# Optimization experiments

Measured on AMD Instinct MI355X. Metric: run time of the kernel, lower is better.

## Reference

```python
import jax, jax.numpy as jnp
import numpy as np

E = 1024
H = 16
D = E // H  # head_dim = 64
B = 2
S = 2048


def setup_inputs() -> dict:
    key = jax.random.key(0)
    ks = jax.random.split(key, 8)
    sc = 0.02
    return {
        "x": jax.random.normal(ks[0], (B, S, E), jnp.float32),
        "rotation_params": jax.random.normal(ks[1], (E, E), jnp.float32) * sc,
        "entangle_params": jax.random.normal(ks[2], (E, E), jnp.float32) * sc,
        "qkv_w": jax.random.normal(ks[3], (3 * E, E), jnp.float32) * sc,
        "qkv_b": jax.random.normal(ks[4], (3 * E,), jnp.float32) * sc,
        "out_w": jax.random.normal(ks[5], (E, E), jnp.float32) * sc,
        "out_b": jax.random.normal(ks[6], (E,), jnp.float32) * sc,
    }


def reference(x, rotation_params, entangle_params, qkv_w, qkv_b, out_w, out_b):
    b, s, _ = x.shape
    # qkv projection (torch Linear: x @ W.T + b)
    qkv = jnp.einsum('bse,fe->bsf', x, qkv_w) + qkv_b
    q, k, v = jnp.split(qkv, 3, axis=-1)
    # extra rotation / entangle matmuls on q and k
    q = jnp.matmul(q, rotation_params)
    k = jnp.matmul(k, entangle_params)
    # split heads: (b, h, s, d)
    q = q.reshape(b, s, H, D).transpose(0, 2, 1, 3)
    k = k.reshape(b, s, H, D).transpose(0, 2, 1, 3)
    v = v.reshape(b, s, H, D).transpose(0, 2, 1, 3)
    scores = jnp.einsum('bhqd,bhkd->bhqk', q, k) / np.sqrt(D).astype(np.float32)
    attn = jax.nn.softmax(scores, axis=-1)  # dropout p=0.0 -> identity
    out = jnp.einsum('bhqk,bhkd->bhqd', attn, v)
    out = out.transpose(0, 2, 1, 3).reshape(b, s, E)
    out = jnp.einsum('bse,fe->bsf', out, out_w) + out_b
    return out + x
```

## Files before the change

kernel.cpp:

```cpp
#include <hip/hip_runtime.h>

#define US unsigned short
#define UC unsigned char

typedef __bf16 bf16x8 __attribute__((ext_vector_type(8)));
typedef float f32x4 __attribute__((ext_vector_type(4)));
typedef unsigned int u32x4 __attribute__((ext_vector_type(4)));
typedef unsigned short u16x4 __attribute__((ext_vector_type(4)));
typedef unsigned int uint2v __attribute__((ext_vector_type(2)));

#define ALPHA_Q 0.180336880111f

#if __has_builtin(__builtin_amdgcn_exp2f)
#define EXP2F(x) __builtin_amdgcn_exp2f(x)
#else
#define EXP2F(x) __expf(0.69314718f * (x))
#endif

static __device__ __forceinline__ US f2bf(float f) {
    union { float f; unsigned u; } v; v.f = f;
    unsigned r = v.u + 0x7fffu + ((v.u >> 16) & 1u);
    return (US)(r >> 16);
}
static __device__ __forceinline__ float bf2f(US h) {
    union { unsigned u; float f; } v; v.u = ((unsigned)h) << 16;
    return v.f;
}
static __device__ __forceinline__ f32x4 mfma16(bf16x8 a, bf16x8 b, f32x4 c) {
    return __builtin_amdgcn_mfma_f32_16x16x32_bf16(a, b, c, 0, 0, 0);
}
static __device__ __forceinline__ f32x4 mfma_fp8(long long a, long long b, f32x4 c) {
    return __builtin_amdgcn_mfma_f32_16x16x32_fp8_fp8(a, b, c, 0, 0, 0);
}
static __device__ __forceinline__ void gload16(const US* g, US* l) {
    __builtin_amdgcn_global_load_lds(
        (const __attribute__((address_space(1))) void*)g,
        (__attribute__((address_space(3))) void*)l, 16, 0, 0);
}
static __device__ __forceinline__ void gload16b(const UC* g, UC* l) {
    __builtin_amdgcn_global_load_lds(
        (const __attribute__((address_space(1))) void*)g,
        (__attribute__((address_space(3))) void*)l, 16, 0, 0);
}
static __device__ __forceinline__ void stf(float* p, float v) { *p = v; }
static __device__ __forceinline__ void stf(US* p, float v) { *p = f2bf(v); }

__global__ __launch_bounds__(256) void prep(
    const float* __restrict__ x, US* __restrict__ xb,
    const float* __restrict__ qkvw, US* __restrict__ wv,
    const float* __restrict__ outw, US* __restrict__ wo,
    const float* __restrict__ Rm, US* __restrict__ rt,
    const float* __restrict__ Em, US* __restrict__ et,
    US* __restrict__ wqT, US* __restrict__ wkT,
    const float* __restrict__ qkvb, float* __restrict__ b3)
{
    __shared__ float t[64][65];
    const int bx = blockIdx.x;
    if (bx < 6144) {
        int i = bx * 256 + threadIdx.x;
        const float* s; US* d; int j;
        if (i < 1048576) { s = x; d = xb; j = i; }
        else if (i < 1310720) { s = qkvw + (size_t)2048 * 1024; d = wv; j = i - 1048576; }
        else { s = outw; d = wo; j = i - 1310720; }
        f32x4 v = ((const f32x4*)s)[j];
        u16x4 o;
        o.x = f2bf(v.x); o.y = f2bf(v.y); o.z = f2bf(v.z); o.w = f2bf(v.w);
        ((u16x4*)d)[j] = o;
    } else if (bx < 7168) {
        int r = bx - 6144;
        int z = r >> 8, xy = r & 255, tbx = xy & 15, tby = xy >> 4;
        const float* ip; US* op;
        switch (z) {
            case 0: ip = Rm; op = rt; break;
            case 1: ip = Em; op = et; break;
            case 2: ip = qkvw; op = wqT; break;
            default: ip = qkvw + (size_t)1024 * 1024; op = wkT; break;
        }
        int bc = tbx * 64, br = tby * 64;
        int lx = threadIdx.x & 63, y4 = threadIdx.x >> 6;
#pragma unroll
        for (int i = 0; i < 16; ++i) {
            int rr = i * 4 + y4;
            t[rr][lx] = ip[(size_t)(br + rr) * 1024 + bc + lx];
        }
        __syncthreads();
#pragma unroll
        for (int i = 0; i < 16; ++i) {
            int c = i * 4 + y4;
            op[(size_t)(bc + c) * 1024 + br + lx] = f2bf(t[lx][c]);
        }
    } else if (bx < 7296) {
        float (*red)[64] = (float(*)[64])t;
        const int bb = bx - 7168;
        const int tid = threadIdx.x, wave = tid >> 6, lane = tid & 63;
        const int nc = bb & 31, jc = bb >> 5;
        const int n0 = nc * 64, n = n0 + lane;
        const float* M = (n0 < 1024) ? Rm : Em;
        const float* bv = qkvb + ((n0 < 1024) ? 0 : 1024);
        const int nn = (n0 < 1024) ? n : n - 1024;
        float s = 0.f;
        const int j0 = jc * 256 + wave * 64;
#pragma unroll 8
        for (int j = 0; j < 64; ++j)
            s += bv[j0 + j] * M[(size_t)(j0 + j) * 1024 + nn];
        red[wave][lane] = s;
        __syncthreads();
        if (wave == 0) {
            float tt = red[0][lane] + red[1][lane] + red[2][lane] + red[3][lane];
            atomicAdd(&b3[n], (n0 < 1024) ? tt * ALPHA_Q : tt);
        }
    } else {
        int i = (bx - 7296) * 256 + threadIdx.x;
        b3[2048 + i] = qkvb[2048 + i];
    }
}

template <typename TO>
__global__ __launch_bounds__(256) void gemm_nt64(
    const US* __restrict__ A, const US* __restrict__ Bm,
    TO* __restrict__ C, const float* __restrict__ bias,
    const float* __restrict__ resid,
    int M, int N, int K, int lda, int ldb, int ldc)
{
    __shared__ __align__(16) US sA[64 * 64];
    __shared__ __align__(16) US sB[128 * 64];
    const int tid = threadIdx.x;
    const int wave = tid >> 6, lane = tid & 63;
    const int r16 = lane & 15, q4 = lane >> 4;
    const int wm = (wave >> 1) * 32, wn = (wave & 1) * 64;
    const int c7 = r16 & 7;

    const int l8 = lane >> 3, lg = (lane & 7) ^ l8;
    const US* aptr = A + (size_t)(blockIdx.x * 64 + wave * 16 + l8) * lda + lg * 8;
    const US* bptr = Bm + (size_t)(blockIdx.y * 128 + wave * 32 + l8) * ldb + lg * 8;

    f32x4 acc[2][4];
#pragma unroll
    for (int i = 0; i < 2; ++i)
#pragma unroll
        for (int j = 0; j < 4; ++j) acc[i][j] = (f32x4){0.f, 0.f, 0.f, 0.f};

    for (int k0 = 0; k0 < K; k0 += 64) {
        gload16(aptr + k0, sA + (wave * 16) * 64);
        gload16(aptr + (size_t)8 * lda + k0, sA + (wave * 16 + 8) * 64);
#pragma unroll
        for (int c = 0; c < 4; ++c)
            gload16(bptr + (size_t)(c * 8) * ldb + k0, sB + (wave * 32 + c * 8) * 64);
        __syncthreads();
        bf16x8 af[2][2], bfr[4][2];
#pragma unroll
        for (int i = 0; i < 2; ++i)
#pragma unroll
            for (int hf = 0; hf < 2; ++hf)
                af[i][hf] = *(const bf16x8*)&sA[(wm + i * 16 + r16) * 64 + ((hf * 4 + q4) ^ c7) * 8];
#pragma unroll
        for (int j = 0; j < 4; ++j)
#pragma unroll
            for (int hf = 0; hf < 2; ++hf)
                bfr[j][hf] = *(const bf16x8*)&sB[(wn + j * 16 + r16) * 64 + ((hf * 4 + q4) ^ c7) * 8];
#pragma unroll
        for (int i = 0; i < 2; ++i)
#pragma unroll
            for (int j = 0; j < 4; ++j) {
                acc[i][j] = mfma16(af[i][0], bfr[j][0], acc[i][j]);
                acc[i][j] = mfma16(af[i][1], bfr[j][1], acc[i][j]);
            }
        __syncthreads();
    }

#pragma unroll
    for (int j = 0; j < 4; ++j) {
        int col = blockIdx.y * 128 + wn + j * 16 + r16;
        float bv = bias ? bias[col] : 0.f;
#pragma unroll
        for (int i = 0; i < 2; ++i) {
#pragma unroll
            for (int rr = 0; rr < 4; ++rr) {
                int row = blockIdx.x * 64 + wm + i * 16 + q4 * 4 + rr;
                float v = acc[i][j][rr] + bv;
                if (resid) v += resid[(size_t)row * ldc + col];
                stf(&C[(size_t)row * ldc + col], v);
            }
        }
    }
}

__global__ __launch_bounds__(256) void gemm_qkv(
    const US* __restrict__ A, const US* __restrict__ Bm,
    const float* __restrict__ bias,
    US* __restrict__ qk, UC* __restrict__ vt)
{
    __shared__ __align__(16) US sA[64 * 64];
    __shared__ __align__(16) US sB[128 * 64];
    const int tid = threadIdx.x;
    const int wave = tid >> 6, lane = tid & 63;
    const int r16 = lane & 15, q4 = lane >> 4;
    const int wm = (wave >> 1) * 32, wn = (wave & 1) * 64;
    const int c7 = r16 & 7;

    const int l8 = lane >> 3, lg = (lane & 7) ^ l8;
    const US* aptr = A + (size_t)(blockIdx.x * 64 + wave * 16 + l8) * 1024 + lg * 8;
    const US* bptr = Bm + (size_t)(blockIdx.y * 128 + wave * 32 + l8) * 1024 + lg * 8;

    f32x4 acc[2][4];
#pragma unroll
    for (int i = 0; i < 2; ++i)
#pragma unroll
        for (int j = 0; j < 4; ++j) acc[i][j] = (f32x4){0.f, 0.f, 0.f, 0.f};

    for (int k0 = 0; k0 < 1024; k0 += 64) {
        gload16(aptr + k0, sA + (wave * 16) * 64);
        gload16(aptr + (size_t)8 * 1024 + k0, sA + (wave * 16 + 8) * 64);
#pragma unroll
        for (int c = 0; c < 4; ++c)
            gload16(bptr + (size_t)(c * 8) * 1024 + k0, sB + (wave * 32 + c * 8) * 64);
        __syncthreads();
        bf16x8 af[2][2], bfr[4][2];
#pragma unroll
        for (int i = 0; i < 2; ++i)
#pragma unroll
            for (int hf = 0; hf < 2; ++hf)
                af[i][hf] = *(const bf16x8*)&sA[(wm + i * 16 + r16) * 64 + ((hf * 4 + q4) ^ c7) * 8];
#pragma unroll
        for (int j = 0; j < 4; ++j)
#pragma unroll
            for (int hf = 0; hf < 2; ++hf)
                bfr[j][hf] = *(const bf16x8*)&sB[(wn + j * 16 + r16) * 64 + ((hf * 4 + q4) ^ c7) * 8];
#pragma unroll
        for (int i = 0; i < 2; ++i)
#pragma unroll
            for (int j = 0; j < 4; ++j) {
                acc[i][j] = mfma16(af[i][0], bfr[j][0], acc[i][j]);
                acc[i][j] = mfma16(af[i][1], bfr[j][1], acc[i][j]);
            }
        __syncthreads();
    }

    if (blockIdx.y < 16) {
#pragma unroll
        for (int j = 0; j < 4; ++j) {
            int col = blockIdx.y * 128 + wn + j * 16 + r16;
            float bv = bias[col];
#pragma unroll
            for (int i = 0; i < 2; ++i)
#pragma unroll
                for (int rr = 0; rr < 4; ++rr) {
                    int row = blockIdx.x * 64 + wm + i * 16 + q4 * 4 + rr;
                    qk[(size_t)row * 2048 + col] = f2bf(acc[i][j][rr] + bv);
                }
        }
    } else {
#pragma unroll
        for (int j = 0; j < 4; ++j) {
            int col = blockIdx.y * 128 + wn + j * 16 + r16;
            float bv = bias[col];
            int f = col - 2048;
#pragma unroll
            for (int i = 0; i < 2; ++i) {
                int row0 = blockIdx.x * 64 + wm + i * 16 + q4 * 4;
                int b = row0 >> 11, s0 = row0 & 2047;
                int k = s0 & 63;
                int p = (s0 & ~63) | ((k & 24) << 1) | ((k & 32) >> 2) | (k & 7);
                int dw = __builtin_amdgcn_cvt_pk_fp8_f32(
                    acc[i][j][0] + bv, acc[i][j][1] + bv, 0, false);
                dw = __builtin_amdgcn_cvt_pk_fp8_f32(
                    acc[i][j][2] + bv, acc[i][j][3] + bv, dw, true);
                *(unsigned int*)&vt[((size_t)(b * 1024 + f)) * 2048 + p] = (unsigned)dw;
            }
        }
    }
}

__global__ __launch_bounds__(256) void gemm_fold(
    const US* __restrict__ rt, const US* __restrict__ wqT,
    const US* __restrict__ et, const US* __restrict__ wkT,
    US* __restrict__ comb)
{
    __shared__ __align__(16) US sA[64 * 32];
    __shared__ __align__(16) US sB[64 * 32];
    const US* A; const US* Bm; US* C; float alpha;
    if (blockIdx.z == 0) { A = rt; Bm = wqT; C = comb; alpha = ALPHA_Q; }
    else { A = et; Bm = wkT; C = comb + (size_t)1024 * 1024; alpha = 1.0f; }

    const int tid = threadIdx.x;
    const int wave = tid >> 6, lane = tid & 63;
    const int r16 = lane & 15, q4 = lane >> 4;
    const int wm = (wave >> 1) * 32, wn = (wave & 1) * 32;

    const int srow = wave * 16 + (lane >> 2);
    const int sg = lane & 3;
    const US* aptr = A + (size_t)(blockIdx.x * 64 + srow) * 1024 + sg * 8;
    const US* bptr = Bm + (size_t)(blockIdx.y * 64 + srow) * 1024 + sg * 8;
    US* lA = sA + (wave * 16) * 32;
    US* lB = sB + (wave * 16) * 32;

    f32x4 acc[2][2];
#pragma unroll
    for (int i = 0; i < 2; ++i)
#pragma unroll
        for (int j = 0; j < 2; ++j) acc[i][j] = (f32x4){0.f, 0.f, 0.f, 0.f};

    for (int k0 = 0; k0 < 1024; k0 += 32) {
        gload16(aptr + k0, lA);
        gload16(bptr + k0, lB);
        __syncthreads();
        bf16x8 af[2], bfr[2];
#pragma unroll
        for (int i = 0; i < 2; ++i)
            af[i] = *(const bf16x8*)&sA[(wm + i * 16 + r16) * 32 + q4 * 8];
#pragma unroll
        for (int j = 0; j < 2; ++j)
            bfr[j] = *(const bf16x8*)&sB[(wn + j * 16 + r16) * 32 + q4 * 8];
#pragma unroll
        for (int i = 0; i < 2; ++i)
#pragma unroll
            for (int j = 0; j < 2; ++j) acc[i][j] = mfma16(af[i], bfr[j], acc[i][j]);
        __syncthreads();
    }

#pragma unroll
    for (int j = 0; j < 2; ++j) {
        int col = blockIdx.y * 64 + wn + j * 16 + r16;
#pragma unroll
        for (int i = 0; i < 2; ++i)
#pragma unroll
            for (int rr = 0; rr < 4; ++rr) {
                int row = blockIdx.x * 64 + wm + i * 16 + q4 * 4 + rr;
                C[(size_t)row * 1024 + col] = f2bf(acc[i][j][rr] * alpha);
            }
    }
}

__global__ __launch_bounds__(256) void attn_kernel(
    const US* __restrict__ qk, const UC* __restrict__ vt, US* __restrict__ out)
{
    __shared__ __align__(16) US sK[2 * 64 * 64];
    __shared__ __align__(16) UC sV[2 * 64 * 64];
    __shared__ __align__(16) UC sP[64 * 72];
    __shared__ float lred[64];
    const int tid = threadIdx.x;
    const int wave = tid >> 6, lane = tid & 63;
    const int r16 = lane & 15, q4 = lane >> 4;
    const int bid = blockIdx.x;
    const int pair = (bid & 7) * 4 + ((bid >> 3) & 3);
    const int qc = bid >> 5;
    const int h = pair & 15, b = pair >> 4;
    const int qrow0 = qc * 64;
    const int c7 = r16 & 7;
    const long long ones8 = 0x3838383838383838LL;

    const US* qbase = qk + ((size_t)(b * 2048 + qrow0)) * 2048 + h * 64;
    bf16x8 qa[4][2];
#pragma unroll
    for (int qt = 0; qt < 4; ++qt)
#pragma unroll
        for (int kh = 0; kh < 2; ++kh)
            qa[qt][kh] = *(const bf16x8*)(qbase + (size_t)(qt * 16 + r16) * 2048 + kh * 32 + q4 * 8);

    f32x4 o[4];
    f32x4 lC;
#pragma unroll
    for (int qt = 0; qt < 4; ++qt) o[qt] = (f32x4){0.f, 0.f, 0.f, 0.f};
    lC = (f32x4){0.f, 0.f, 0.f, 0.f};

    const int l8 = lane >> 3;
    const US* kg = qk + ((size_t)(b * 2048 + wave * 16 + l8)) * 2048 + 1024 + h * 64
                 + ((lane & 7) ^ l8) * 8;
    const int r4 = lane >> 2;
    const UC* vg = vt + ((size_t)((b * 16 + h) * 64 + wave * 16 + r4)) * 2048
                 + ((lane & 3) ^ (r4 & 3)) * 16;

#define STAGE(kc, buf) do {                                                    \
        US* dK = sK + (buf) * 4096 + (wave * 16) * 64;                         \
        UC* dV = sV + (buf) * 4096 + (wave * 16) * 64;                         \
        gload16(kg + (size_t)(kc) * 2048, dK);                                 \
        gload16(kg + (size_t)((kc) + 8) * 2048, dK + 8 * 64);                  \
        gload16b(vg + (kc), dV);                                               \
    } while (0)

    STAGE(0, 0);
    for (int it = 0; it < 32; ++it) {
        const int buf = it & 1;
        asm volatile("s_waitcnt vmcnt(0)" ::: "memory");
        asm volatile("s_barrier" ::: "memory");
        if (it < 31) STAGE((it + 1) * 64, buf ^ 1);

        const US* K0 = sK + buf * 4096;
        bf16x8 kf0 = *(const bf16x8*)&K0[(wave * 16 + r16) * 64 + ((0 + q4) ^ c7) * 8];
        bf16x8 kf1 = *(const bf16x8*)&K0[(wave * 16 + r16) * 64 + ((4 + q4) ^ c7) * 8];
#pragma unroll
        for (int qt = 0; qt < 4; ++qt) {
            f32x4 st = mfma16(kf0, qa[qt][0], (f32x4){0.f, 0.f, 0.f, 0.f});
            st = mfma16(kf1, qa[qt][1], st);
            float p0 = EXP2F(st[0]), p1 = EXP2F(st[1]);
            float p2 = EXP2F(st[2]), p3 = EXP2F(st[3]);
            int dw = __builtin_amdgcn_cvt_pk_fp8_f32(p0, p1, 0, false);
            dw = __builtin_amdgcn_cvt_pk_fp8_f32(p2, p3, dw, true);
            *(unsigned int*)&sP[(qt * 16 + r16) * 72 + wave * 16 + q4 * 4] = (unsigned)dw;
        }
        asm volatile("s_waitcnt lgkmcnt(0)" ::: "memory");
        asm volatile("s_barrier" ::: "memory");

        const UC* V0 = sV + buf * 4096;
        u32x4 vv = *(const u32x4*)&V0[(wave * 16 + r16) * 64 + (q4 ^ (r16 & 3)) * 16];
        long long vf0, vf1;
        { uint2v t0 = {vv.x, vv.y}; vf0 = *(long long*)&t0; }
        { uint2v t1 = {vv.z, vv.w}; vf1 = *(long long*)&t1; }
#pragma unroll
        for (int qt = 0; qt < 4; ++qt) {
            long long pa0 = *(const long long*)&sP[(qt * 16 + r16) * 72 + q4 * 8];
            long long pa1 = *(const long long*)&sP[(qt * 16 + r16) * 72 + 32 + q4 * 8];
            o[qt] = mfma_fp8(vf0, pa0, o[qt]);
            o[qt] = mfma_fp8(vf1, pa1, o[qt]);
        }
        {
            long long pl0 = *(const long long*)&sP[(wave * 16 + r16) * 72 + q4 * 8];
            long long pl1 = *(const long long*)&sP[(wave * 16 + r16) * 72 + 32 + q4 * 8];
            lC = mfma_fp8(ones8, pl0, lC);
            lC = mfma_fp8(ones8, pl1, lC);
        }
    }
#undef STAGE

    if (q4 == 0) lred[wave * 16 + r16] = lC[0];
    __syncthreads();
#pragma unroll
    for (int qt = 0; qt < 4; ++qt) {
        float inv = 1.0f / lred[qt * 16 + r16];
        size_t row = (size_t)(b * 2048 + qrow0 + qt * 16 + r16);
        uint2v w;
        w.x = (unsigned)f2bf(o[qt][0] * inv) | ((unsigned)f2bf(o[qt][1] * inv) << 16);
        w.y = (unsigned)f2bf(o[qt][2] * inv) | ((unsigned)f2bf(o[qt][3] * inv) << 16);
        *(uint2v*)&out[row * 1024 + h * 64 + wave * 16 + q4 * 4] = w;
    }
}

extern "C" void kernel_launch(void* const* d_in, const int* in_sizes, int n_in,
                              void* d_out, int out_size, void* d_ws, size_t ws_size,
                              hipStream_t stream)
{
    const float* x    = (const float*)d_in[0];
    const float* Rm   = (const float*)d_in[1];
    const float* Em   = (const float*)d_in[2];
    const float* qkvw = (const float*)d_in[3];
    const float* qkvb = (const float*)d_in[4];
    const float* outw = (const float*)d_in[5];
    const float* outb = (const float*)d_in[6];
    float* outp = (float*)d_out;

    US* ws    = (US*)d_ws;
    US* xb    = ws;
    US* rt    = xb   + (size_t)4096 * 1024;
    US* et    = rt   + (size_t)1024 * 1024;
    US* wqT   = et   + (size_t)1024 * 1024;
    US* wkT   = wqT  + (size_t)1024 * 1024;
    US* wo    = wkT  + (size_t)1024 * 1024;
    US* comb  = wo   + (size_t)1024 * 1024;
    US* qkvq  = comb + (size_t)3072 * 1024;
    US* ao    = qkvq + (size_t)4096 * 2048;
    UC* vt    = (UC*)(ao + (size_t)4096 * 1024);
    float* b3 = (float*)(vt + (size_t)2048 * 2048);

    hipMemsetAsync(b3, 0, 2048 * sizeof(float), stream);
    prep<<<dim3(7300), dim3(256), 0, stream>>>(
        x, xb, qkvw, comb + (size_t)2048 * 1024, outw, wo,
        Rm, rt, Em, et, wqT, wkT, qkvb, b3);
    gemm_fold<<<dim3(16, 16, 2), dim3(256), 0, stream>>>(rt, wqT, et, wkT, comb);
    gemm_qkv<<<dim3(64, 24), dim3(256), 0, stream>>>(xb, comb, b3, qkvq, vt);
    attn_kernel<<<dim3(1024), dim3(256), 0, stream>>>(qkvq, vt, ao);
    gemm_nt64<float><<<dim3(64, 8), dim3(256), 0, stream>>>(ao, wo, outp, outb, x,
                                                            4096, 1024, 1024, 1024, 1024, 1024);
}
```

Before: 212.1 us.

## Software-pipeline attention loop so QK of one tile overlaps PV of the previous

Restructures the attention main loop into two phases: the QK-score/exp/fp8-pack phase for tile it runs alongside the P·V and row-sum MFMA phase for tile it-1. The P buffer is double-buffered, and K and V staging are split so each is prefetched at a different stage. This cuts the per-iteration barriers from two to one and lets the MFMA and exp work of adjacent tiles interleave. In exchange it uses more LDS for P, adds prologue and epilogue code, and relies on __syncthreads covering the async LDS loads.

```diff
diff --git a/kernel.cpp b/kernel.cpp
--- a/kernel.cpp
+++ b/kernel.cpp
@@ -336,7 +336,7 @@
 {
     __shared__ __align__(16) US sK[2 * 64 * 64];
     __shared__ __align__(16) UC sV[2 * 64 * 64];
-    __shared__ __align__(16) UC sP[64 * 72];
+    __shared__ __align__(16) UC sP[2 * 64 * 72];
     __shared__ float lred[64];
     const int tid = threadIdx.x;
     const int wave = tid >> 6, lane = tid & 63;
@@ -370,57 +370,77 @@
     const UC* vg = vt + ((size_t)((b * 16 + h) * 64 + wave * 16 + r4)) * 2048
                  + ((lane & 3) ^ (r4 & 3)) * 16;
 
-#define STAGE(kc, buf) do {                                                    \
+#define STAGE_K(kc, buf) do {                                                  \
         US* dK = sK + (buf) * 4096 + (wave * 16) * 64;                         \
-        UC* dV = sV + (buf) * 4096 + (wave * 16) * 64;                         \
         gload16(kg + (size_t)(kc) * 2048, dK);                                 \
         gload16(kg + (size_t)((kc) + 8) * 2048, dK + 8 * 64);                  \
+    } while (0)
+#define STAGE_V(kc, buf) do {                                                  \
+        UC* dV = sV + (buf) * 4096 + (wave * 16) * 64;                         \
         gload16b(vg + (kc), dV);                                               \
     } while (0)
 
-    STAGE(0, 0);
-    for (int it = 0; it < 32; ++it) {
-        const int buf = it & 1;
-        asm volatile("s_waitcnt vmcnt(0)" ::: "memory");
-        asm volatile("s_barrier" ::: "memory");
-        if (it < 31) STAGE((it + 1) * 64, buf ^ 1);
-
-        const US* K0 = sK + buf * 4096;
-        bf16x8 kf0 = *(const bf16x8*)&K0[(wave * 16 + r16) * 64 + ((0 + q4) ^ c7) * 8];
-        bf16x8 kf1 = *(const bf16x8*)&K0[(wave * 16 + r16) * 64 + ((4 + q4) ^ c7) * 8];
-#pragma unroll
-        for (int qt = 0; qt < 4; ++qt) {
-            f32x4 st = mfma16(kf0, qa[qt][0], (f32x4){0.f, 0.f, 0.f, 0.f});
-            st = mfma16(kf1, qa[qt][1], st);
-            float p0 = EXP2F(st[0]), p1 = EXP2F(st[1]);
-            float p2 = EXP2F(st[2]), p3 = EXP2F(st[3]);
-            int dw = __builtin_amdgcn_cvt_pk_fp8_f32(p0, p1, 0, false);
-            dw = __builtin_amdgcn_cvt_pk_fp8_f32(p2, p3, dw, true);
-            *(unsigned int*)&sP[(qt * 16 + r16) * 72 + wave * 16 + q4 * 4] = (unsigned)dw;
-        }
-        asm volatile("s_waitcnt lgkmcnt(0)" ::: "memory");
-        asm volatile("s_barrier" ::: "memory");
-
-        const UC* V0 = sV + buf * 4096;
-        u32x4 vv = *(const u32x4*)&V0[(wave * 16 + r16) * 64 + (q4 ^ (r16 & 3)) * 16];
-        long long vf0, vf1;
-        { uint2v t0 = {vv.x, vv.y}; vf0 = *(long long*)&t0; }
-        { uint2v t1 = {vv.z, vv.w}; vf1 = *(long long*)&t1; }
-#pragma unroll
-        for (int qt = 0; qt < 4; ++qt) {
-            long long pa0 = *(const long long*)&sP[(qt * 16 + r16) * 72 + q4 * 8];
-            long long pa1 = *(const long long*)&sP[(qt * 16 + r16) * 72 + 32 + q4 * 8];
-            o[qt] = mfma_fp8(vf0, pa0, o[qt]);
-            o[qt] = mfma_fp8(vf1, pa1, o[qt]);
-        }
-        {
-            long long pl0 = *(const long long*)&sP[(wave * 16 + r16) * 72 + q4 * 8];
-            long long pl1 = *(const long long*)&sP[(wave * 16 + r16) * 72 + 32 + q4 * 8];
-            lC = mfma_fp8(ones8, pl0, lC);
-            lC = mfma_fp8(ones8, pl1, lC);
-        }
-    }
-#undef STAGE
+#define PHASE1(cur) do {                                                       \
+        const US* K0 = sK + (cur) * 4096;                                      \
+        UC* P0 = sP + (cur) * 4608;                                            \
+        bf16x8 kf0 = *(const bf16x8*)&K0[(wave * 16 + r16) * 64 + ((0 + q4) ^ c7) * 8]; \
+        bf16x8 kf1 = *(const bf16x8*)&K0[(wave * 16 + r16) * 64 + ((4 + q4) ^ c7) * 8]; \
+        _Pragma("unroll")                                                      \
+        for (int qt = 0; qt < 4; ++qt) {                                       \
+            f32x4 st = mfma16(kf0, qa[qt][0], (f32x4){0.f, 0.f, 0.f, 0.f});    \
+            st = mfma16(kf1, qa[qt][1], st);                                   \
+            float p0 = EXP2F(st[0]), p1 = EXP2F(st[1]);                        \
+            float p2 = EXP2F(st[2]), p3 = EXP2F(st[3]);                        \
+            int dw = __builtin_amdgcn_cvt_pk_fp8_f32(p0, p1, 0, false);        \
+            dw = __builtin_amdgcn_cvt_pk_fp8_f32(p2, p3, dw, true);            \
+            *(unsigned int*)&P0[(qt * 16 + r16) * 72 + wave * 16 + q4 * 4] = (unsigned)dw; \
+        }                                                                      \
+    } while (0)
+
+#define PHASE2(prv) do {                                                       \
+        const UC* V0 = sV + (prv) * 4096;                                      \
+        const UC* P0 = sP + (prv) * 4608;                                      \
+        u32x4 vv = *(const u32x4*)&V0[(wave * 16 + r16) * 64 + (q4 ^ (r16 & 3)) * 16]; \
+        long long vf0, vf1;                                                    \
+        { uint2v t0 = {vv.x, vv.y}; vf0 = *(long long*)&t0; }                  \
+        { uint2v t1 = {vv.z, vv.w}; vf1 = *(long long*)&t1; }                  \
+        _Pragma("unroll")                                                      \
+        for (int qt = 0; qt < 4; ++qt) {                                       \
+            long long pa0 = *(const long long*)&P0[(qt * 16 + r16) * 72 + q4 * 8];      \
+            long long pa1 = *(const long long*)&P0[(qt * 16 + r16) * 72 + 32 + q4 * 8]; \
+            o[qt] = mfma_fp8(vf0, pa0, o[qt]);                                 \
+            o[qt] = mfma_fp8(vf1, pa1, o[qt]);                                 \
+        }                                                                      \
+        {                                                                      \
+            long long pl0 = *(const long long*)&P0[(wave * 16 + r16) * 72 + q4 * 8];    \
+            long long pl1 = *(const long long*)&P0[(wave * 16 + r16) * 72 + 32 + q4 * 8]; \
+            lC = mfma_fp8(ones8, pl0, lC);                                     \
+            lC = mfma_fp8(ones8, pl1, lC);                                     \
+        }                                                                      \
+    } while (0)
+
+    STAGE_K(0, 0);
+    __syncthreads();
+    STAGE_K(64, 1);
+    STAGE_V(0, 0);
+    PHASE1(0);
+
+#pragma unroll 2
+    for (int it = 1; it < 32; ++it) {
+        const int cur = it & 1;
+        __syncthreads();
+        if (it < 31) STAGE_K((it + 1) * 64, cur ^ 1);
+        STAGE_V(it * 64, cur);
+        PHASE1(cur);
+        PHASE2(cur ^ 1);
+    }
+    __syncthreads();
+    PHASE2(1);
+
+#undef STAGE_K
+#undef STAGE_V
+#undef PHASE1
+#undef PHASE2
 
     if (q4 == 0) lred[wave * 16 + r16] = lC[0];
     __syncthreads();
```

Measured after the change: 211.7 us. About the same (-0.2%).
